# Optimization experiments

Measured on AMD Instinct MI355X. Metric: run time of the kernel, lower is better.

The kernel has to match this reference:

```python
import jax, jax.numpy as jnp
import numpy as np
from jax import lax

B, L, M, H = 8, 16, 256, 53
HID, NH, HD = 64, 4, 16  # hidden_size, n_heads, head_dim
ACT = 15  # 3 sub-actions x 5 categories


def _lstm_last(x, Wih, Whh, bih, bhh):
    # x: [N, T, D] batch_first; torch LSTM gate order i,f,g,o. Returns last hidden [N, HID].
    N = x.shape[0]
    h0 = jnp.zeros((N, HID), x.dtype)
    c0 = jnp.zeros((N, HID), x.dtype)
    def step(carry, xt):
        h, c = carry
        g = xt @ Wih.T + bih + h @ Whh.T + bhh
        i, f, gg, o = jnp.split(g, 4, axis=-1)
        c = jax.nn.sigmoid(f) * c + jax.nn.sigmoid(i) * jnp.tanh(gg)
        h = jax.nn.sigmoid(o) * jnp.tanh(c)
        return (h, c), None
    (h, _), _ = lax.scan(step, (h0, c0), x.transpose(1, 0, 2))
    return h


def setup_inputs():
    key = jax.random.key(0)
    ks = jax.random.split(key, 32)
    rn = lambda k, sh: (jax.random.normal(k, sh, jnp.float32) * 0.05)
    Gmat = jax.random.randint(ks[3], (M, M), 0, 2)
    Gmat = Gmat.at[jnp.arange(M), jnp.arange(M)].set(1)  # self-contact so no all-masked row
    return {
        'x_actor': jax.random.normal(ks[0], (B, L, M, H), jnp.float32),
        'x_critic': jax.random.normal(ks[1], (B, L, M, H), jnp.float32),
        'action': jax.random.randint(ks[2], (B, M, 3), 0, 5),
        'Gmat': Gmat,
        'Wa': rn(ks[4], (HID, H)), 'ba': jnp.zeros((HID,), jnp.float32),
        'Wg': rn(ks[5], (HID, H)), 'bg': jnp.zeros((HID,), jnp.float32),
        'Qw': rn(ks[6], (HID, HID)), 'Kw': rn(ks[7], (HID, HID)),
        'W2': rn(ks[8], (HID, 2 * HID)), 'b2': jnp.zeros((HID,), jnp.float32),
        'Wih_a': rn(ks[9], (4 * HID, HID)), 'Whh_a': rn(ks[10], (4 * HID, HID)),
        'bih_a': jnp.zeros((4 * HID,), jnp.float32), 'bhh_a': jnp.zeros((4 * HID,), jnp.float32),
        'Wih_c': rn(ks[11], (4 * HID, HID)), 'Whh_c': rn(ks[12], (4 * HID, HID)),
        'bih_c': jnp.zeros((4 * HID,), jnp.float32), 'bhh_c': jnp.zeros((4 * HID,), jnp.float32),
        'Wma1': rn(ks[13], (HID, HID)), 'bma1': jnp.zeros((HID,), jnp.float32),
        'Wma2': rn(ks[14], (ACT, HID)), 'bma2': jnp.zeros((ACT,), jnp.float32),
        'Wmc1': rn(ks[15], (HID, HID)), 'bmc1': jnp.zeros((HID,), jnp.float32),
        'Wmc2': rn(ks[16], (1, HID)), 'bmc2': jnp.zeros((1,), jnp.float32),
    }


def reference(x_actor, x_critic, action, Gmat, Wa, ba, Wg, bg, Qw, Kw, W2, b2,
              Wih_a, Whh_a, bih_a, bhh_a, Wih_c, Whh_c, bih_c, bhh_c,
              Wma1, bma1, Wma2, bma2, Wmc1, bmc1, Wmc2, bmc2):
    Bb, Ll, Mm, Hh = x_actor.shape
    xa = x_actor.transpose(1, 0, 2, 3).reshape(Ll * Bb, Mm, Hh)
    xc = xa  # original code overwrites x_critic with x_actor (preserved)
    a_lin = xa @ Wa.T + ba                               # [LB, M, HID]
    # --- GAT (GCN2) ---
    s = xc @ Wg.T + bg                                   # [LB, M, HID]
    q = (s @ Qw).reshape(-1, Mm, NH, HD)
    k = (s @ Kw).reshape(-1, Mm, NH, HD)
    s4 = s.reshape(-1, Mm, NH, HD)
    att = jnp.einsum('blhe,bshe->bhls', q, k) / jnp.asarray(128.0, s.dtype) ** 0.5
    att = jnp.where(Gmat > 0, att, jnp.asarray(-9e15, att.dtype))
    att = jax.nn.softmax(att, axis=-1)
    s_out = jnp.einsum('bshe,bhls->blhe', s4, att).reshape(-1, Mm, NH * HD)
    c_feat = jnp.concatenate([s, s_out], axis=-1) @ W2.T + b2  # [LB, M, HID]
    # --- to sequences [B*M, L, HID] ---
    xa_seq = a_lin.reshape(Ll, Bb * Mm, HID).transpose(1, 0, 2)
    xc_seq = c_feat.reshape(Ll, Bb * Mm, HID).transpose(1, 0, 2)
    ah = _lstm_last(xa_seq, Wih_a, Whh_a, bih_a, bhh_a)          # [B*M, HID]
    ch = _lstm_last(xc_seq, Wih_c, Whh_c, bih_c, bhh_c).reshape(Bb, Mm, HID)
    logits = (jnp.tanh(ah @ Wma1.T + bma1) @ Wma2.T + bma2).reshape(Bb, Mm, 3, 5)
    logp = jax.nn.log_softmax(logits, axis=-1)
    lp = jnp.take_along_axis(logp, action[..., None], axis=-1).squeeze(-1)  # [B,M,3]
    ent = -jnp.sum(jnp.exp(logp) * logp, axis=-1)                           # [B,M,3]
    value = jnp.tanh(ch @ Wmc1.T + bmc1) @ Wmc2.T + bmc2                    # [B,M,1]
    return (action, lp.sum(-1), ent.sum(-1), value)
```

## Files before the change

### kernel.cpp

```cpp
#include <hip/hip_runtime.h>
#include <math.h>

#define B_ 8
#define L_ 16
#define M_ 256
#define H_ 53
#define HID_ 64
#define LB_ 128
#define SCALE_ 0.08838834764831845f

typedef __attribute__((ext_vector_type(8))) short bf16x8;
typedef __attribute__((ext_vector_type(4))) float f32x4;

__device__ inline unsigned short f2bf(float f) {
  unsigned u = __builtin_bit_cast(unsigned, f);
  unsigned r = (u + 0x7FFFu + ((u >> 16) & 1u)) >> 16;
  return (unsigned short)r;
}
__device__ inline float bf2f(unsigned short u) {
  unsigned v = ((unsigned)u) << 16;
  return __builtin_bit_cast(float, v);
}
__device__ inline float sigm(float x) { return __builtin_amdgcn_rcpf(1.f + __expf(-x)); }
__device__ inline float ftanh(float x) { return 1.f - 2.f * __builtin_amdgcn_rcpf(1.f + __expf(2.f * x)); }

__global__ __launch_bounds__(256) void kP_pre(
    const float* __restrict__ Wa, const float* __restrict__ Wg,
    const float* __restrict__ bg,
    const float* __restrict__ Qw, const float* __restrict__ Kw,
    unsigned short* __restrict__ WQ_b, unsigned short* __restrict__ WK_b,
    float* __restrict__ bqk, unsigned short* __restrict__ Wab_b) {
  int blk = blockIdx.x, tid = threadIdx.x;
  if (blk < 32) {
    int idx = blk * 256 + tid;
    int which = idx >> 12, n = (idx >> 6) & 63, j = idx & 63;
    const float* Mm = which ? Kw : Qw;
    float acc = 0.f;
    if (j < 53) {
      for (int e = 0; e < 64; ++e) acc = fmaf(Mm[e * 64 + n], Wg[e * 53 + j], acc);
      if (which == 0) acc *= SCALE_;
    }
    (which ? WK_b : WQ_b)[n * 64 + j] = f2bf(acc);
  } else if (blk == 32) {
    if (tid < 128) {
      int which = tid >> 6, n = tid & 63;
      const float* Mm = which ? Kw : Qw;
      float acc = 0.f;
      for (int e = 0; e < 64; ++e) acc = fmaf(bg[e], Mm[e * 64 + n], acc);
      if (which == 0) acc *= SCALE_;
      bqk[tid] = acc;
    }
  } else {
    int base = (blk - 33) * 4096;
    #pragma unroll
    for (int k = 0; k < 16; ++k) {
      int idx = base + k * 256 + tid;
      int n = idx >> 6, j = idx & 63;
      float v = 0.f;
      if (j < 53) v = (n < 64) ? Wa[n * 53 + j] : Wg[(n - 64) * 53 + j];
      Wab_b[idx] = f2bf(v);
    }
  }
}

#define WS 68
#define OS 268
__global__ __launch_bounds__(256, 2) void kA_lin(const float* __restrict__ x,
    const unsigned short* __restrict__ Wab_b,
    const unsigned short* __restrict__ WQ_b, const unsigned short* __restrict__ WK_b,
    const float* __restrict__ ba, const float* __restrict__ bg,
    const float* __restrict__ bqk,
    const int* __restrict__ Gmat, const float* __restrict__ Wih_c,
    const float* __restrict__ W2, const float* __restrict__ b2,
    const float* __restrict__ Whh_a, const float* __restrict__ Whh_c,
    const float* __restrict__ Wih_a,
    unsigned short* __restrict__ a_lin_bf, unsigned short* __restrict__ s_b,
    unsigned short* __restrict__ q_b, unsigned short* __restrict__ k_b,
    unsigned short* __restrict__ sT_b,
    unsigned short* __restrict__ Wfold_b, float* __restrict__ bias_fold,
    unsigned* __restrict__ gmask,
    unsigned short* __restrict__ Whha_b, unsigned short* __restrict__ Whhc_b,
    unsigned short* __restrict__ Wiha_b) {
  int tid = threadIdx.x, blk = blockIdx.x;
  if (blk >= 512) {
    int b2k = blk - 512;
    if (b2k < 128) {
      int idx = b2k * 256 + tid;
      int n = idx >> 7, t = idx & 127;
      float acc = 0.f;
      for (int e = 0; e < 64; ++e) acc = fmaf(Wih_c[n * 64 + e], W2[e * 128 + t], acc);
      Wfold_b[idx] = f2bf(acc);
    } else if (b2k < 192) {
      int l = (b2k - 128) * 4 + (tid >> 6);
      int ln = tid & 63;
      #pragma unroll
      for (int c = 0; c < 4; ++c) {
        int gv = Gmat[l * 256 + c * 64 + ln];
        unsigned long long msk = __ballot(gv > 0);
        if (ln == 0) {
          gmask[l * 8 + c * 2] = (unsigned)msk;
          gmask[l * 8 + c * 2 + 1] = (unsigned)(msk >> 32);
        }
      }
    } else if (b2k == 192) {
      float acc = 0.f;
      for (int e = 0; e < 64; ++e) acc = fmaf(Wih_c[tid * 64 + e], b2[e], acc);
      bias_fold[tid] = acc;
    } else {
      int base = (b2k - 193) * 2048;
      #pragma unroll
      for (int k = 0; k < 8; ++k) {
        int idx = base + k * 256 + tid;
        if (idx < 16384) Whha_b[idx] = f2bf(Whh_a[idx]);
        else if (idx < 32768) Whhc_b[idx - 16384] = f2bf(Whh_c[idx - 16384]);
        else Wiha_b[idx - 32768] = f2bf(Wih_a[idx - 32768]);
      }
    }
    return;
  }
  __shared__ __attribute__((aligned(16))) char smem[70144];
  float* x_raw = (float*)smem;
  unsigned short* out_lds = (unsigned short*)smem;
  unsigned short* w_lds = (unsigned short*)(smem + 34304);
  float* bias_lds = (float*)(smem + 69120);
  int row0 = blk * 64;
  int lbA = row0 >> 8, m0 = row0 & 255;
  int lA = lbA >> 3, bA = lbA & 7;
  {
    const uint4* xs = (const uint4*)(x + ((bA * L_ + lA) * M_ + m0) * H_);
    uint4* xr = (uint4*)x_raw;
    #pragma unroll
    for (int k = 0; k < 4; ++k) {
      int i = k * 256 + tid;
      if (i < 848) xr[i] = xs[i];
    }
  }
  #pragma unroll
  for (int k = 0; k < 8; ++k) {
    int i = k * 256 + tid;
    int n = i >> 3, c8 = (i & 7) * 8;
    const unsigned short* src = n < 128 ? Wab_b + n * 64
                              : (n < 192 ? WQ_b + (n - 128) * 64 : WK_b + (n - 192) * 64);
    *(uint4*)&w_lds[n * WS + c8] = *(const uint4*)(src + c8);
  }
  {
    float bv;
    if (tid < 64) bv = ba[tid];
    else if (tid < 128) bv = bg[tid - 64];
    else bv = bqk[tid - 128];
    bias_lds[tid] = bv;
  }
  __syncthreads();
  int lane = tid & 63, w = tid >> 6;
  int c16 = lane & 15, q4 = lane >> 4;
  int lrow = w * 16 + c16;
  bf16x8 a0, a1;
  #pragma unroll
  for (int e = 0; e < 8; ++e)
    a0[e] = (short)f2bf(x_raw[lrow * H_ + q4 * 8 + e]);
  #pragma unroll
  for (int e = 0; e < 8; ++e) {
    int c = 32 + q4 * 8 + e;
    a1[e] = (c < H_) ? (short)f2bf(x_raw[lrow * H_ + c]) : (short)0;
  }
  __syncthreads();
  #pragma unroll
  for (int nt = 0; nt < 16; ++nt) {
    bf16x8 b0 = *(const bf16x8*)&w_lds[(nt * 16 + c16) * WS + q4 * 8];
    bf16x8 b1 = *(const bf16x8*)&w_lds[(nt * 16 + c16) * WS + 32 + q4 * 8];
    float bs = bias_lds[nt * 16 + c16];
    f32x4 acc = {bs, bs, bs, bs};
    acc = __builtin_amdgcn_mfma_f32_16x16x32_bf16(a0, b0, acc, 0, 0, 0);
    acc = __builtin_amdgcn_mfma_f32_16x16x32_bf16(a1, b1, acc, 0, 0, 0);
    #pragma unroll
    for (int rr = 0; rr < 4; ++rr)
      out_lds[(w * 16 + q4 * 4 + rr) * OS + nt * 16 + c16] = f2bf(acc[rr]);
  }
  __syncthreads();
  #pragma unroll
  for (int k = 0; k < 8; ++k) {
    int i = k * 256 + tid;
    int r = i >> 5, seg = i & 31;
    int which = seg >> 3, n8 = (seg & 7) * 8;
    uint4 v = *(const uint4*)&out_lds[r * OS + which * 64 + n8];
    unsigned short* dst = which == 0 ? a_lin_bf : which == 1 ? s_b : which == 2 ? q_b : k_b;
    *(uint4*)&dst[(row0 + r) * 64 + n8] = v;
  }
  #pragma unroll
  for (int k = 0; k < 4; ++k) {
    int i = k * 256 + tid;
    int e = i >> 4, mc = i & 15;
    ushort4 v;
    v.x = out_lds[(mc * 4 + 0) * OS + 64 + e];
    v.y = out_lds[(mc * 4 + 1) * OS + 64 + e];
    v.z = out_lds[(mc * 4 + 2) * OS + 64 + e];
    v.w = out_lds[(mc * 4 + 3) * OS + 64 + e];
    *(ushort4*)&sT_b[(lbA * 64 + e) * 256 + m0 + mc * 4] = v;
  }
}

__global__ __launch_bounds__(512, 4) void kB_attn(
    const unsigned short* __restrict__ qb, const unsigned short* __restrict__ kb,
    const unsigned short* __restrict__ sT, const unsigned* __restrict__ gmask,
    unsigned short* __restrict__ so_b) {
  __shared__ __attribute__((aligned(16))) unsigned short k_lds[256 * 68];
  __shared__ __attribute__((aligned(16))) unsigned short sT_lds[64 * 280];
  int bid = blockIdx.x;
  int xcd = bid & 7;
  int rest = bid >> 3;
  int l0 = (rest & 3) << 6;
  int lb = (rest >> 2) * 8 + xcd;
  int tid = threadIdx.x;
  int kbase = lb * 256;
  for (int i = tid; i < 2048; i += 512) {
    int s = i >> 3, e8 = (i & 7) * 8;
    *(uint4*)&k_lds[s * 68 + e8] = *(const uint4*)(kb + (kbase + s) * 64 + e8);
  }
  for (int i = tid; i < 2048; i += 512) {
    int e = i >> 5, m8 = (i & 31) * 8;
    *(uint4*)&sT_lds[e * 280 + m8] = *(const uint4*)(sT + (lb * 64 + e) * 256 + m8);
  }
  int lane = tid & 63, w = tid >> 6;
  int c16 = lane & 15, q4 = lane >> 4;
  int lrow0 = (w >> 1) * 16;
  int h0 = (w & 1) * 2;
  int lrow = lb * 256 + l0 + lrow0;
  const bf16x8 z8 = {0, 0, 0, 0, 0, 0, 0, 0};
  bf16x8 bq[2];
  #pragma unroll
  for (int hp = 0; hp < 2; ++hp) {
    int h = h0 + hp;
    bq[hp] = (q4 < 2) ? *(const bf16x8*)(qb + (lrow + c16) * 64 + h * 16 + q4 * 8) : z8;
  }
  unsigned gwv[8];
  #pragma unroll
  for (int sp = 0; sp < 8; ++sp) gwv[sp] = gmask[(l0 + lrow0 + c16) * 8 + sp];
  __syncthreads();
  f32x4 accO[2];
  float sumh[2];
  #pragma unroll
  for (int hp = 0; hp < 2; ++hp) { accO[hp] = (f32x4){0.f, 0.f, 0.f, 0.f}; sumh[hp] = 0.f; }

  #pragma unroll
  for (int sp = 0; sp < 8; ++sp) {
    unsigned gw = gwv[sp];
    #pragma unroll
    for (int hp = 0; hp < 2; ++hp) {
      int h = h0 + hp;
      unsigned pk0A, pk1A, pk0B, pk1B;
      #pragma unroll
      for (int tp = 0; tp < 2; ++tp) {
        int t = sp * 2 + tp;
        bf16x8 ka = z8;
        if (q4 < 2) ka = *(const bf16x8*)&k_lds[(t * 16 + c16) * 68 + h * 16 + q4 * 8];
        f32x4 d = __builtin_amdgcn_mfma_f32_16x16x32_bf16(ka, bq[hp], (f32x4){0.f, 0.f, 0.f, 0.f}, 0, 0, 0);
        int bitbase = tp * 16 + q4 * 4;
        float p0 = ((gw >> (bitbase + 0)) & 1u) ? __expf(d[0]) : 0.f;
        float p1 = ((gw >> (bitbase + 1)) & 1u) ? __expf(d[1]) : 0.f;
        float p2 = ((gw >> (bitbase + 2)) & 1u) ? __expf(d[2]) : 0.f;
        float p3 = ((gw >> (bitbase + 3)) & 1u) ? __expf(d[3]) : 0.f;
        sumh[hp] += (p0 + p1) + (p2 + p3);
        unsigned lo = (unsigned)f2bf(p0) | ((unsigned)f2bf(p1) << 16);
        unsigned hi = (unsigned)f2bf(p2) | ((unsigned)f2bf(p3) << 16);
        if (tp == 0) { pk0A = lo; pk1A = hi; } else { pk0B = lo; pk1B = hi; }
      }
      int srcA = ((q4 & 1) * 2) * 16 + c16, srcB = srcA + 16;
      unsigned g0A = (unsigned)__shfl((int)pk0A, srcA);
      unsigned g1A = (unsigned)__shfl((int)pk1A, srcA);
      unsigned g2A = (unsigned)__shfl((int)pk0A, srcB);
      unsigned g3A = (unsigned)__shfl((int)pk1A, srcB);
      unsigned g0B = (unsigned)__shfl((int)pk0B, srcA);
      unsigned g1B = (unsigned)__shfl((int)pk1B, srcA);
      unsigned g2B = (unsigned)__shfl((int)pk0B, srcB);
      unsigned g3B = (unsigned)__shfl((int)pk1B, srcB);
      bool useB = (q4 >= 2);
      uint4 av;
      av.x = useB ? g0B : g0A;
      av.y = useB ? g1B : g1A;
      av.z = useB ? g2B : g2A;
      av.w = useB ? g3B : g3A;
      bf16x8 af = __builtin_bit_cast(bf16x8, av);
      bf16x8 bs = *(const bf16x8*)&sT_lds[(h * 16 + c16) * 280 + sp * 32 + q4 * 8];
      accO[hp] = __builtin_amdgcn_mfma_f32_16x16x32_bf16(af, bs, accO[hp], 0, 0, 0);
    }
  }
  #pragma unroll
  for (int hp = 0; hp < 2; ++hp) {
    int h = h0 + hp;
    float s = sumh[hp];
    s += __shfl_xor(s, 16);
    s += __shfl_xor(s, 32);
    #pragma unroll
    for (int r = 0; r < 4; ++r) {
      float sv = __shfl(s, q4 * 4 + r);
      float o = accO[hp][r] / sv;
      so_b[(lb * 256 + l0 + lrow0 + q4 * 4 + r) * 64 + h * 16 + c16] = f2bf(o);
    }
  }
}

__global__ __launch_bounds__(256, 1) void kR_lstm(
    const unsigned short* __restrict__ a_lin_bf,
    const unsigned short* __restrict__ s_b, const unsigned short* __restrict__ so_b,
    const unsigned short* __restrict__ Wfold_b, const float* __restrict__ bias_fold,
    const unsigned short* __restrict__ Wiha_b,
    const unsigned short* __restrict__ Whha_b, const unsigned short* __restrict__ Whhc_b,
    const float* __restrict__ bih_a, const float* __restrict__ bhh_a,
    const float* __restrict__ bih_c, const float* __restrict__ bhh_c,
    const int* __restrict__ action,
    const float* __restrict__ Wma1, const float* __restrict__ bma1,
    const float* __restrict__ Wma2, const float* __restrict__ bma2,
    const float* __restrict__ Wmc1, const float* __restrict__ bmc1,
    const float* __restrict__ Wmc2, const float* __restrict__ bmc2,
    float* __restrict__ out) {
  int blk = blockIdx.x;
  int which = blk >> 7, g = blk & 127;
  int seq0 = g * 16;
  int b = seq0 >> 8, m0 = seq0 & 255;
  __shared__ __attribute__((aligned(16))) unsigned short h_lds[2][16][72];
  __shared__ __attribute__((aligned(16))) unsigned short ha_lds[16][72];
  __shared__ float logit_lds[16][16];
  __shared__ float grp_lds[16][8];
  __shared__ float val_lds[16][4];
  int tid = threadIdx.x;
  int lane = tid & 63, w = tid >> 6;
  int c16 = lane & 15, q4 = lane >> 4;
  int hs0 = w * 16;
  const unsigned short* Whh_b = which ? Whhc_b : Whha_b;
  const float* bih = which ? bih_c : bih_a;
  const float* bhh = which ? bhh_c : bhh_a;
  bf16x8 bwhh[4][2];
  float bias[4];
  #pragma unroll
  for (int nt = 0; nt < 4; ++nt) {
    int n = nt * 64 + hs0 + c16;
    bias[nt] = bih[n] + bhh[n] + (which ? bias_fold[n] : 0.f);
    #pragma unroll
    for (int kf = 0; kf < 2; ++kf)
      bwhh[nt][kf] = *(const bf16x8*)(Whh_b + n * 64 + kf * 32 + q4 * 8);
  }
  for (int i = tid; i < 576; i += 256) ((unsigned*)h_lds)[i] = 0u;
  float cr[4] = {0.f, 0.f, 0.f, 0.f};
  const int STEP = 2048 * 64;
  __syncthreads();
  int cur = 0;
  if (which == 0) {
    bf16x8 bwin[4][2];
    #pragma unroll
    for (int nt = 0; nt < 4; ++nt) {
      int n = nt * 64 + hs0 + c16;
      #pragma unroll
      for (int kf = 0; kf < 2; ++kf)
        bwin[nt][kf] = *(const bf16x8*)(Wiha_b + n * 64 + kf * 32 + q4 * 8);
    }
    const unsigned short* inb = a_lin_bf + (b * 256 + m0 + c16) * 64;
    bf16x8 i0c = *(const bf16x8*)(inb + q4 * 8);
    bf16x8 i1c = *(const bf16x8*)(inb + 32 + q4 * 8);
    for (int l = 0; l < L_; ++l) {
      bf16x8 i0n = i0c, i1n = i1c;
      if (l < L_ - 1) {
        i0n = *(const bf16x8*)(inb + (l + 1) * STEP + q4 * 8);
        i1n = *(const bf16x8*)(inb + (l + 1) * STEP + 32 + q4 * 8);
      }
      bf16x8 ah0 = *(const bf16x8*)&h_lds[cur][c16][q4 * 8];
      bf16x8 ah1 = *(const bf16x8*)&h_lds[cur][c16][32 + q4 * 8];
      f32x4 acc[4];
      #pragma unroll
      for (int nt = 0; nt < 4; ++nt) {
        f32x4 a = {bias[nt], bias[nt], bias[nt], bias[nt]};
        a = __builtin_amdgcn_mfma_f32_16x16x32_bf16(i0c, bwin[nt][0], a, 0, 0, 0);
        a = __builtin_amdgcn_mfma_f32_16x16x32_bf16(i1c, bwin[nt][1], a, 0, 0, 0);
        a = __builtin_amdgcn_mfma_f32_16x16x32_bf16(ah0, bwhh[nt][0], a, 0, 0, 0);
        a = __builtin_amdgcn_mfma_f32_16x16x32_bf16(ah1, bwhh[nt][1], a, 0, 0, 0);
        acc[nt] = a;
      }
      #pragma unroll
      for (int rr = 0; rr < 4; ++rr) {
        float si = sigm(acc[0][rr]);
        float sf = sigm(acc[1][rr]);
        float gg = ftanh(acc[2][rr]);
        float so_ = sigm(acc[3][rr]);
        cr[rr] = sf * cr[rr] + si * gg;
        float hvv = so_ * ftanh(cr[rr]);
        h_lds[cur ^ 1][q4 * 4 + rr][hs0 + c16] = f2bf(hvv);
      }
      __syncthreads();
      cur ^= 1;
      i0c = i0n; i1c = i1n;
    }
  } else {
    bf16x8 bwf[4][4];
    #pragma unroll
    for (int nt = 0; nt < 4; ++nt) {
      int n = nt * 64 + hs0 + c16;
      #pragma unroll
// ... 40 lines not shown
      }
      __syncthreads();
      cur ^= 1;
      s0c = s0n; s1c = s1n; o0c = o0n; o1c = o1n;
    }
  }
  bf16x8 fh0 = *(const bf16x8*)&h_lds[cur][c16][q4 * 8];
  bf16x8 fh1 = *(const bf16x8*)&h_lds[cur][c16][32 + q4 * 8];
  if (which == 0) {
    bf16x8 bm1[2];
    #pragma unroll
    for (int kf = 0; kf < 2; ++kf) {
      const float* wp = Wma1 + (hs0 + c16) * 64 + kf * 32 + q4 * 8;
      bf16x8 bb;
      #pragma unroll
      for (int j = 0; j < 8; ++j) bb[j] = (short)f2bf(wp[j]);
      bm1[kf] = bb;
    }
    float bs = bma1[hs0 + c16];
    f32x4 acc = {bs, bs, bs, bs};
    acc = __builtin_amdgcn_mfma_f32_16x16x32_bf16(fh0, bm1[0], acc, 0, 0, 0);
    acc = __builtin_amdgcn_mfma_f32_16x16x32_bf16(fh1, bm1[1], acc, 0, 0, 0);
    #pragma unroll
    for (int rr = 0; rr < 4; ++rr)
      ha_lds[q4 * 4 + rr][hs0 + c16] = f2bf(ftanh(acc[rr]));
    __syncthreads();
    if (w == 0) {
      bf16x8 af0 = *(const bf16x8*)&ha_lds[c16][q4 * 8];
      bf16x8 af1 = *(const bf16x8*)&ha_lds[c16][32 + q4 * 8];
      const bf16x8 z8 = {0, 0, 0, 0, 0, 0, 0, 0};
      bf16x8 bw2[2] = {z8, z8};
      float bs2 = 0.f;
      if (c16 < 15) {
        #pragma unroll
        for (int kf = 0; kf < 2; ++kf) {
          const float* wp = Wma2 + c16 * 64 + kf * 32 + q4 * 8;
          bf16x8 bb;
          #pragma unroll
          for (int j = 0; j < 8; ++j) bb[j] = (short)f2bf(wp[j]);
          bw2[kf] = bb;
        }
        bs2 = bma2[c16];
      }
      f32x4 acc2 = {bs2, bs2, bs2, bs2};
      acc2 = __builtin_amdgcn_mfma_f32_16x16x32_bf16(af0, bw2[0], acc2, 0, 0, 0);
      acc2 = __builtin_amdgcn_mfma_f32_16x16x32_bf16(af1, bw2[1], acc2, 0, 0, 0);
      #pragma unroll
      for (int rr = 0; rr < 4; ++rr)
        logit_lds[q4 * 4 + rr][c16] = acc2[rr];
    }
    __syncthreads();
    if (tid < 48) {
      int useq = tid & 15, t = tid >> 4;
      int n = seq0 + useq;
      float l0 = logit_lds[useq][t * 5 + 0], l1 = logit_lds[useq][t * 5 + 1];
      float l2 = logit_lds[useq][t * 5 + 2], l3 = logit_lds[useq][t * 5 + 3];
      float l4 = logit_lds[useq][t * 5 + 4];
      float mx = fmaxf(fmaxf(fmaxf(l0, l1), fmaxf(l2, l3)), l4);
      float sm = __expf(l0 - mx) + __expf(l1 - mx) + __expf(l2 - mx) +
                 __expf(l3 - mx) + __expf(l4 - mx);
      float lse = __logf(sm) + mx;
      int a = action[n * 3 + t];
      float lp0 = l0 - lse, lp1 = l1 - lse, lp2 = l2 - lse, lp3 = l3 - lse, lp4 = l4 - lse;
      float lpsel = logit_lds[useq][t * 5 + a] - lse;
      float ent = -(__expf(lp0) * lp0 + __expf(lp1) * lp1 + __expf(lp2) * lp2 +
                    __expf(lp3) * lp3 + __expf(lp4) * lp4);
      grp_lds[useq][t] = lpsel;
      grp_lds[useq][4 + t] = ent;
      out[n * 3 + t] = (float)a;
    }
    __syncthreads();
    if (tid < 16) {
      int n = seq0 + tid;
      out[6144 + n] = grp_lds[tid][0] + grp_lds[tid][1] + grp_lds[tid][2];
      out[8192 + n] = grp_lds[tid][4] + grp_lds[tid][5] + grp_lds[tid][6];
    }
  } else {
    bf16x8 bm1[2];
    #pragma unroll
    for (int kf = 0; kf < 2; ++kf) {
      const float* wp = Wmc1 + (hs0 + c16) * 64 + kf * 32 + q4 * 8;
      bf16x8 bb;
      #pragma unroll
      for (int j = 0; j < 8; ++j) bb[j] = (short)f2bf(wp[j]);
      bm1[kf] = bb;
    }
    float bs = bmc1[hs0 + c16];
    f32x4 acc = {bs, bs, bs, bs};
    acc = __builtin_amdgcn_mfma_f32_16x16x32_bf16(fh0, bm1[0], acc, 0, 0, 0);
    acc = __builtin_amdgcn_mfma_f32_16x16x32_bf16(fh1, bm1[1], acc, 0, 0, 0);
    float wv2 = Wmc2[hs0 + c16];
    float pv[4];
    #pragma unroll
    for (int rr = 0; rr < 4; ++rr) pv[rr] = ftanh(acc[rr]) * wv2;
    #pragma unroll
    for (int rr = 0; rr < 4; ++rr) {
      pv[rr] += __shfl_xor(pv[rr], 1);
      pv[rr] += __shfl_xor(pv[rr], 2);
      pv[rr] += __shfl_xor(pv[rr], 4);
      pv[rr] += __shfl_xor(pv[rr], 8);
    }
    if (c16 == 0) {
      #pragma unroll
      for (int rr = 0; rr < 4; ++rr) val_lds[q4 * 4 + rr][w] = pv[rr];
    }
    __syncthreads();
    if (tid < 16) {
      int n = seq0 + tid;
      out[10240 + n] = val_lds[tid][0] + val_lds[tid][1] + val_lds[tid][2] +
                       val_lds[tid][3] + bmc2[0];
    }
  }
}

extern "C" void kernel_launch(void* const* d_in, const int* in_sizes, int n_in,
                              void* d_out, int out_size, void* d_ws, size_t ws_size,
                              hipStream_t stream) {
  const float* x_actor = (const float*)d_in[0];
  const int* action = (const int*)d_in[2];
  const int* Gmat  = (const int*)d_in[3];
  const float* Wa = (const float*)d_in[4];  const float* ba = (const float*)d_in[5];
  const float* Wg = (const float*)d_in[6];  const float* bg = (const float*)d_in[7];
  const float* Qw = (const float*)d_in[8];  const float* Kw = (const float*)d_in[9];
  const float* W2 = (const float*)d_in[10]; const float* b2 = (const float*)d_in[11];
  const float* Wih_a = (const float*)d_in[12]; const float* Whh_a = (const float*)d_in[13];
  const float* bih_a = (const float*)d_in[14]; const float* bhh_a = (const float*)d_in[15];
  const float* Wih_c = (const float*)d_in[16]; const float* Whh_c = (const float*)d_in[17];
  const float* bih_c = (const float*)d_in[18]; const float* bhh_c = (const float*)d_in[19];
  const float* Wma1 = (const float*)d_in[20]; const float* bma1 = (const float*)d_in[21];
  const float* Wma2 = (const float*)d_in[22]; const float* bma2 = (const float*)d_in[23];
  const float* Wmc1 = (const float*)d_in[24]; const float* bmc1 = (const float*)d_in[25];
  const float* Wmc2 = (const float*)d_in[26]; const float* bmc2 = (const float*)d_in[27];

  unsigned short* us = (unsigned short*)d_ws;
  unsigned short* a_lin_bf = us;
  unsigned short* s_b  = us + 2097152;
  unsigned short* q_b  = us + 4194304;
  unsigned short* k_b  = us + 6291456;
  unsigned short* sT_b = us + 8388608;
  unsigned short* so_b = us + 10485760;
  unsigned short* Wfold_b = us + 12582912;
  unsigned short* Whha_b  = us + 12615680;
  unsigned short* Whhc_b  = us + 12632064;
  unsigned short* Wiha_b  = us + 12648448;
  unsigned short* WQ_b    = us + 12664832;
  unsigned short* WK_b    = us + 12668928;
  unsigned short* Wab_b   = us + 12673024;
  float* fb = (float*)(us + 12681216);
  float* bias_fold = fb;
  float* bqk = fb + 256;
  unsigned* gmask = (unsigned*)(fb + 384);
  float* out = (float*)d_out;

  kP_pre<<<35, 256, 0, stream>>>(Wa, Wg, bg, Qw, Kw, WQ_b, WK_b, bqk, Wab_b);
  kA_lin<<<729, 256, 0, stream>>>(x_actor, Wab_b, WQ_b, WK_b, ba, bg, bqk,
                                  Gmat, Wih_c, W2, b2, Whh_a, Whh_c, Wih_a,
                                  a_lin_bf, s_b, q_b, k_b, sT_b,
                                  Wfold_b, bias_fold, gmask,
                                  Whha_b, Whhc_b, Wiha_b);
  kB_attn<<<512, 512, 0, stream>>>(q_b, k_b, sT_b, gmask, so_b);
  kR_lstm<<<256, 256, 0, stream>>>(a_lin_bf, s_b, so_b, Wfold_b, bias_fold,
                                   Wiha_b, Whha_b, Whhc_b,
                                   bih_a, bhh_a, bih_c, bhh_c,
                                   action, Wma1, bma1, Wma2, bma2,
                                   Wmc1, bmc1, Wmc2, bmc2, out);
}
```

Before: 67.94 us.

## Fuse all four kernels into one cooperative megakernel with grid syncs

Replaces the four-kernel launch sequence with a single cooperative kernel of 256 blocks x 512 threads that runs the same stages (weight prep, input projection, masked attention, LSTM plus heads) separated by grid.sync barriers. The aim is to remove launch gaps and inter-kernel drain between stages. The trade-offs are fewer resident blocks than the separate launches used (729 and 512 blocks before), idle half-blocks in the prep and LSTM stages, and the cost of the grid barriers themselves. The old multi-kernel path is kept as a fallback if the cooperative launch fails.

```diff
diff --git a/kernel.cpp b/kernel.cpp
--- a/kernel.cpp
+++ b/kernel.cpp
@@ -1,5 +1,8 @@
 #include <hip/hip_runtime.h>
+#include <hip/hip_cooperative_groups.h>
 #include <math.h>
+
+namespace cg = cooperative_groups;
 
 #define B_ 8
 #define L_ 16
@@ -23,6 +26,522 @@
 }
 __device__ inline float sigm(float x) { return __builtin_amdgcn_rcpf(1.f + __expf(-x)); }
 __device__ inline float ftanh(float x) { return 1.f - 2.f * __builtin_amdgcn_rcpf(1.f + __expf(2.f * x)); }
+
+__global__ __launch_bounds__(512, 2) void kMega(
+    const float* __restrict__ x,
+    const float* __restrict__ Wa, const float* __restrict__ Wg,
+    const float* __restrict__ ba, const float* __restrict__ bg,
+    const float* __restrict__ Qw, const float* __restrict__ Kw,
+    const int* __restrict__ Gmat, const float* __restrict__ Wih_c,
+    const float* __restrict__ W2, const float* __restrict__ b2,
+    const float* __restrict__ Whh_a, const float* __restrict__ Whh_c,
+    const float* __restrict__ Wih_a,
+    const float* __restrict__ bih_a, const float* __restrict__ bhh_a,
+    const float* __restrict__ bih_c, const float* __restrict__ bhh_c,
+    const int* __restrict__ action,
+    const float* __restrict__ Wma1, const float* __restrict__ bma1,
+    const float* __restrict__ Wma2, const float* __restrict__ bma2,
+    const float* __restrict__ Wmc1, const float* __restrict__ bmc1,
+    const float* __restrict__ Wmc2, const float* __restrict__ bmc2,
+    unsigned short* __restrict__ WQ_b, unsigned short* __restrict__ WK_b,
+    float* __restrict__ bqk, unsigned short* __restrict__ Wab_b,
+    unsigned short* __restrict__ a_lin_bf, unsigned short* __restrict__ s_b,
+    unsigned short* __restrict__ q_b, unsigned short* __restrict__ k_b,
+    unsigned short* __restrict__ sT_b, unsigned short* __restrict__ so_b,
+    unsigned short* __restrict__ Wfold_b, float* __restrict__ bias_fold,
+    unsigned* __restrict__ gmask,
+    unsigned short* __restrict__ Whha_b, unsigned short* __restrict__ Whhc_b,
+    unsigned short* __restrict__ Wiha_b, float* __restrict__ out) {
+  __shared__ __attribute__((aligned(16))) char smem[140288];
+  cg::grid_group grid = cg::this_grid();
+  int blk = blockIdx.x, tid = threadIdx.x;
+
+  if (tid < 256) {
+    int t = tid;
+    if (blk < 32) {
+      int idx = blk * 256 + t;
+      int which = idx >> 12, n = (idx >> 6) & 63, j = idx & 63;
+      const float* Mm = which ? Kw : Qw;
+      float acc = 0.f;
+      if (j < 53) {
+        for (int e = 0; e < 64; ++e) acc = fmaf(Mm[e * 64 + n], Wg[e * 53 + j], acc);
+        if (which == 0) acc *= SCALE_;
+      }
+      (which ? WK_b : WQ_b)[n * 64 + j] = f2bf(acc);
+    } else if (blk == 32) {
+      if (t < 128) {
+        int which = t >> 6, n = t & 63;
+        const float* Mm = which ? Kw : Qw;
+        float acc = 0.f;
+        for (int e = 0; e < 64; ++e) acc = fmaf(bg[e], Mm[e * 64 + n], acc);
+        if (which == 0) acc *= SCALE_;
+        bqk[t] = acc;
+      }
+      float bacc = 0.f;
+      for (int e = 0; e < 64; ++e) bacc = fmaf(Wih_c[t * 64 + e], b2[e], bacc);
+      bias_fold[t] = bacc;
+    } else if (blk < 35) {
+      int base = (blk - 33) * 4096;
+      #pragma unroll
+      for (int k = 0; k < 16; ++k) {
+        int idx = base + k * 256 + t;
+        int n = idx >> 6, j = idx & 63;
+        float v = 0.f;
+        if (j < 53) v = (n < 64) ? Wa[n * 53 + j] : Wg[(n - 64) * 53 + j];
+        Wab_b[idx] = f2bf(v);
+      }
+    } else if (blk < 163) {
+      int idx = (blk - 35) * 256 + t;
+      int n = idx >> 7, tt = idx & 127;
+      float acc = 0.f;
+      for (int e = 0; e < 64; ++e) acc = fmaf(Wih_c[n * 64 + e], W2[e * 128 + tt], acc);
+      Wfold_b[idx] = f2bf(acc);
+    } else if (blk < 227) {
+      int l = (blk - 163) * 4 + (t >> 6);
+      int ln = t & 63;
+      #pragma unroll
+      for (int c = 0; c < 4; ++c) {
+        int gv = Gmat[l * 256 + c * 64 + ln];
+        unsigned long long msk = __ballot(gv > 0);
+        if (ln == 0) {
+          gmask[l * 8 + c * 2] = (unsigned)msk;
+          gmask[l * 8 + c * 2 + 1] = (unsigned)(msk >> 32);
+        }
+      }
+    } else if (blk < 251) {
+      int base = (blk - 227) * 2048;
+      #pragma unroll
+      for (int k = 0; k < 8; ++k) {
+        int idx = base + k * 256 + t;
+        if (idx < 16384) Whha_b[idx] = f2bf(Whh_a[idx]);
+        else if (idx < 32768) Whhc_b[idx - 16384] = f2bf(Whh_c[idx - 16384]);
+        else Wiha_b[idx - 32768] = f2bf(Wih_a[idx - 32768]);
+      }
+    }
+  }
+  grid.sync();
+
+  {
+    int group = tid >> 8, t = tid & 255;
+    char* base = smem + group * 70144;
+    float* x_raw = (float*)base;
+    unsigned short* out_lds = (unsigned short*)base;
+    unsigned short* w_lds = (unsigned short*)(base + 34304);
+    float* bias_lds = (float*)(base + 69120);
+    int job = blk * 2 + group;
+    int row0 = job * 64;
+    int lbA = row0 >> 8, m0 = row0 & 255;
+    int lA = lbA >> 3, bA = lbA & 7;
+    {
+      const uint4* xs = (const uint4*)(x + ((bA * L_ + lA) * M_ + m0) * H_);
+      uint4* xr = (uint4*)x_raw;
+      #pragma unroll
+      for (int k = 0; k < 4; ++k) {
+        int i = k * 256 + t;
+        if (i < 848) xr[i] = xs[i];
+      }
+    }
+    #pragma unroll
+    for (int k = 0; k < 8; ++k) {
+      int i = k * 256 + t;
+      int n = i >> 3, c8 = (i & 7) * 8;
+      const unsigned short* src = n < 128 ? Wab_b + n * 64
+                                : (n < 192 ? WQ_b + (n - 128) * 64 : WK_b + (n - 192) * 64);
+      *(uint4*)&w_lds[n * 68 + c8] = *(const uint4*)(src + c8);
+    }
+    {
+      float bv;
+      if (t < 64) bv = ba[t];
+      else if (t < 128) bv = bg[t - 64];
+      else bv = bqk[t - 128];
+      bias_lds[t] = bv;
+    }
+    __syncthreads();
+    int lane = t & 63, w = t >> 6;
+    int c16 = lane & 15, q4 = lane >> 4;
+    int lrow = w * 16 + c16;
+    bf16x8 a0, a1;
+    #pragma unroll
+    for (int e = 0; e < 8; ++e)
+      a0[e] = (short)f2bf(x_raw[lrow * H_ + q4 * 8 + e]);
+    #pragma unroll
+    for (int e = 0; e < 8; ++e) {
+      int c = 32 + q4 * 8 + e;
+      a1[e] = (c < H_) ? (short)f2bf(x_raw[lrow * H_ + c]) : (short)0;
+    }
+    __syncthreads();
+    #pragma unroll
+    for (int nt = 0; nt < 16; ++nt) {
+      bf16x8 b0 = *(const bf16x8*)&w_lds[(nt * 16 + c16) * 68 + q4 * 8];
+      bf16x8 b1 = *(const bf16x8*)&w_lds[(nt * 16 + c16) * 68 + 32 + q4 * 8];
+      float bs = bias_lds[nt * 16 + c16];
+      f32x4 acc = {bs, bs, bs, bs};
+      acc = __builtin_amdgcn_mfma_f32_16x16x32_bf16(a0, b0, acc, 0, 0, 0);
+      acc = __builtin_amdgcn_mfma_f32_16x16x32_bf16(a1, b1, acc, 0, 0, 0);
+      #pragma unroll
+      for (int rr = 0; rr < 4; ++rr)
+        out_lds[(w * 16 + q4 * 4 + rr) * 268 + nt * 16 + c16] = f2bf(acc[rr]);
+    }
+    __syncthreads();
+    #pragma unroll
+    for (int k = 0; k < 8; ++k) {
+      int i = k * 256 + t;
+      int r = i >> 5, seg = i & 31;
+      int which = seg >> 3, n8 = (seg & 7) * 8;
+      uint4 v = *(const uint4*)&out_lds[r * 268 + which * 64 + n8];
+      unsigned short* dst = which == 0 ? a_lin_bf : which == 1 ? s_b : which == 2 ? q_b : k_b;
+      *(uint4*)&dst[(row0 + r) * 64 + n8] = v;
+    }
+    #pragma unroll
+    for (int k = 0; k < 4; ++k) {
+      int i = k * 256 + t;
+      int e = i >> 4, mc = i & 15;
+      ushort4 v;
+      v.x = out_lds[(mc * 4 + 0) * 268 + 64 + e];
+      v.y = out_lds[(mc * 4 + 1) * 268 + 64 + e];
+      v.z = out_lds[(mc * 4 + 2) * 268 + 64 + e];
+      v.w = out_lds[(mc * 4 + 3) * 268 + 64 + e];
+      *(ushort4*)&sT_b[(lbA * 64 + e) * 256 + m0 + mc * 4] = v;
+    }
+  }
+  grid.sync();
+
+  {
+    unsigned short* k_lds = (unsigned short*)smem;
+    unsigned short* sT_lds = (unsigned short*)(smem + 34816);
+    int lb = blk >> 1, half = blk & 1;
+    int kbase = lb * 256;
+    for (int i = tid; i < 2048; i += 512) {
+      int s = i >> 3, e8 = (i & 7) * 8;
+      *(uint4*)&k_lds[s * 68 + e8] = *(const uint4*)(k_b + (kbase + s) * 64 + e8);
+    }
+    for (int i = tid; i < 2048; i += 512) {
+      int e = i >> 5, m8 = (i & 31) * 8;
+      *(uint4*)&sT_lds[e * 280 + m8] = *(const uint4*)(sT_b + (lb * 64 + e) * 256 + m8);
+    }
+    __syncthreads();
+    int lane = tid & 63, w = tid >> 6;
+    int c16 = lane & 15, q4 = lane >> 4;
+    int lrow0 = (w >> 1) * 16;
+    int h0 = (w & 1) * 2;
+    const bf16x8 z8 = {0, 0, 0, 0, 0, 0, 0, 0};
+    #pragma unroll
+    for (int q2 = 0; q2 < 2; ++q2) {
+      int l0 = ((half << 1) | q2) << 6;
+      int lrow = lb * 256 + l0 + lrow0;
+      bf16x8 bq[2];
+      #pragma unroll
+      for (int hp = 0; hp < 2; ++hp) {
+        int h = h0 + hp;
+        bq[hp] = (q4 < 2) ? *(const bf16x8*)(q_b + (lrow + c16) * 64 + h * 16 + q4 * 8) : z8;
+      }
+      unsigned gwv[8];
+      #pragma unroll
+      for (int sp = 0; sp < 8; ++sp) gwv[sp] = gmask[(l0 + lrow0 + c16) * 8 + sp];
+      f32x4 accO[2];
+      float sumh[2];
+      #pragma unroll
+      for (int hp = 0; hp < 2; ++hp) { accO[hp] = (f32x4){0.f, 0.f, 0.f, 0.f}; sumh[hp] = 0.f; }
+      #pragma unroll
+      for (int sp = 0; sp < 8; ++sp) {
+        unsigned gw = gwv[sp];
+        #pragma unroll
+        for (int hp = 0; hp < 2; ++hp) {
+          int h = h0 + hp;
+          unsigned pk0A, pk1A, pk0B, pk1B;
+          #pragma unroll
+          for (int tp = 0; tp < 2; ++tp) {
+            int tt = sp * 2 + tp;
+            bf16x8 ka = z8;
+            if (q4 < 2) ka = *(const bf16x8*)&k_lds[(tt * 16 + c16) * 68 + h * 16 + q4 * 8];
+            f32x4 d = __builtin_amdgcn_mfma_f32_16x16x32_bf16(ka, bq[hp], (f32x4){0.f, 0.f, 0.f, 0.f}, 0, 0, 0);
+            int bitbase = tp * 16 + q4 * 4;
+            float p0 = ((gw >> (bitbase + 0)) & 1u) ? __expf(d[0]) : 0.f;
+            float p1 = ((gw >> (bitbase + 1)) & 1u) ? __expf(d[1]) : 0.f;
+            float p2 = ((gw >> (bitbase + 2)) & 1u) ? __expf(d[2]) : 0.f;
+            float p3 = ((gw >> (bitbase + 3)) & 1u) ? __expf(d[3]) : 0.f;
+            sumh[hp] += (p0 + p1) + (p2 + p3);
+            unsigned lo = (unsigned)f2bf(p0) | ((unsigned)f2bf(p1) << 16);
+            unsigned hi = (unsigned)f2bf(p2) | ((unsigned)f2bf(p3) << 16);
+            if (tp == 0) { pk0A = lo; pk1A = hi; } else { pk0B = lo; pk1B = hi; }
+          }
+          int srcA = ((q4 & 1) * 2) * 16 + c16, srcB = srcA + 16;
+          unsigned g0A = (unsigned)__shfl((int)pk0A, srcA);
+          unsigned g1A = (unsigned)__shfl((int)pk1A, srcA);
+          unsigned g2A = (unsigned)__shfl((int)pk0A, srcB);
+          unsigned g3A = (unsigned)__shfl((int)pk1A, srcB);
+          unsigned g0B = (unsigned)__shfl((int)pk0B, srcA);
+          unsigned g1B = (unsigned)__shfl((int)pk1B, srcA);
+          unsigned g2B = (unsigned)__shfl((int)pk0B, srcB);
+          unsigned g3B = (unsigned)__shfl((int)pk1B, srcB);
+          bool useB = (q4 >= 2);
+          uint4 av;
+          av.x = useB ? g0B : g0A;
+          av.y = useB ? g1B : g1A;
+          av.z = useB ? g2B : g2A;
+          av.w = useB ? g3B : g3A;
+          bf16x8 af = __builtin_bit_cast(bf16x8, av);
+          bf16x8 bs = *(const bf16x8*)&sT_lds[(h * 16 + c16) * 280 + sp * 32 + q4 * 8];
+          accO[hp] = __builtin_amdgcn_mfma_f32_16x16x32_bf16(af, bs, accO[hp], 0, 0, 0);
+        }
+      }
+      #pragma unroll
+      for (int hp = 0; hp < 2; ++hp) {
+        int h = h0 + hp;
+        float s = sumh[hp];
+        s += __shfl_xor(s, 16);
+        s += __shfl_xor(s, 32);
+        #pragma unroll
+        for (int r = 0; r < 4; ++r) {
+          float sv = __shfl(s, q4 * 4 + r);
+          float o = accO[hp][r] / sv;
+          so_b[(lb * 256 + l0 + lrow0 + q4 * 4 + r) * 64 + h * 16 + c16] = f2bf(o);
+        }
+      }
+    }
+  }
+  grid.sync();
+
+  if (tid < 256) {
+    int t = tid;
+    unsigned short (*h_lds)[16][72] = (unsigned short(*)[16][72])(smem);
+    unsigned short (*ha_lds)[72] = (unsigned short(*)[72])(smem + 4608);
+    float (*logit_lds)[16] = (float(*)[16])(smem + 6912);
+    float (*grp_lds)[8] = (float(*)[8])(smem + 7936);
+    float (*val_lds)[4] = (float(*)[4])(smem + 8448);
+    int which = blk >> 7, g = blk & 127;
+    int seq0 = g * 16;
+    int b = seq0 >> 8, m0 = seq0 & 255;
+    int lane = t & 63, w = t >> 6;
+    int c16 = lane & 15, q4 = lane >> 4;
+    int hs0 = w * 16;
+    const unsigned short* Whh_bp = which ? Whhc_b : Whha_b;
+    const float* bih = which ? bih_c : bih_a;
+    const float* bhh = which ? bhh_c : bhh_a;
+    bf16x8 bwhh[4][2];
+    float bias[4];
+    #pragma unroll
+    for (int nt = 0; nt < 4; ++nt) {
+      int n = nt * 64 + hs0 + c16;
+      bias[nt] = bih[n] + bhh[n] + (which ? bias_fold[n] : 0.f);
+      #pragma unroll
+      for (int kf = 0; kf < 2; ++kf)
+        bwhh[nt][kf] = *(const bf16x8*)(Whh_bp + n * 64 + kf * 32 + q4 * 8);
+    }
+    for (int i = t; i < 576; i += 256) ((unsigned*)smem)[i] = 0u;
+    float cr[4] = {0.f, 0.f, 0.f, 0.f};
+    float hv[4] = {0.f, 0.f, 0.f, 0.f};
+    const int STEP = 2048 * 64;
+    __syncthreads();
+    int cur = 0;
+    if (which == 0) {
+      bf16x8 bwin[4][2];
+      #pragma unroll
+      for (int nt = 0; nt < 4; ++nt) {
+        int n = nt * 64 + hs0 + c16;
+        #pragma unroll
+        for (int kf = 0; kf < 2; ++kf)
+          bwin[nt][kf] = *(const bf16x8*)(Wiha_b + n * 64 + kf * 32 + q4 * 8);
+      }
+      const unsigned short* inb = a_lin_bf + (b * 256 + m0 + c16) * 64;
+      bf16x8 i0c = *(const bf16x8*)(inb + q4 * 8);
+      bf16x8 i1c = *(const bf16x8*)(inb + 32 + q4 * 8);
+      for (int l = 0; l < L_; ++l) {
+        bf16x8 i0n = i0c, i1n = i1c;
+        if (l < L_ - 1) {
+          i0n = *(const bf16x8*)(inb + (l + 1) * STEP + q4 * 8);
+          i1n = *(const bf16x8*)(inb + (l + 1) * STEP + 32 + q4 * 8);
+        }
+        bf16x8 ah0 = *(const bf16x8*)&h_lds[cur][c16][q4 * 8];
+        bf16x8 ah1 = *(const bf16x8*)&h_lds[cur][c16][32 + q4 * 8];
+        f32x4 acc[4];
+        #pragma unroll
+        for (int nt = 0; nt < 4; ++nt) {
+          f32x4 a = {bias[nt], bias[nt], bias[nt], bias[nt]};
+          a = __builtin_amdgcn_mfma_f32_16x16x32_bf16(i0c, bwin[nt][0], a, 0, 0, 0);
+          a = __builtin_amdgcn_mfma_f32_16x16x32_bf16(i1c, bwin[nt][1], a, 0, 0, 0);
+          a = __builtin_amdgcn_mfma_f32_16x16x32_bf16(ah0, bwhh[nt][0], a, 0, 0, 0);
+          a = __builtin_amdgcn_mfma_f32_16x16x32_bf16(ah1, bwhh[nt][1], a, 0, 0, 0);
+          acc[nt] = a;
+        }
+        #pragma unroll
+        for (int rr = 0; rr < 4; ++rr) {
+          float si = sigm(acc[0][rr]);
+          float sf = sigm(acc[1][rr]);
+          float gg = ftanh(acc[2][rr]);
+          float so_ = sigm(acc[3][rr]);
+          cr[rr] = sf * cr[rr] + si * gg;
+          hv[rr] = so_ * ftanh(cr[rr]);
+          h_lds[cur ^ 1][q4 * 4 + rr][hs0 + c16] = f2bf(hv[rr]);
+        }
+        __syncthreads();
+        cur ^= 1;
+        i0c = i0n; i1c = i1n;
+      }
+    } else {
+      bf16x8 bwf[4][4];
+      #pragma unroll
+      for (int nt = 0; nt < 4; ++nt) {
+        int n = nt * 64 + hs0 + c16;
+        #pragma unroll
+        for (int kc = 0; kc < 4; ++kc)
+          bwf[nt][kc] = *(const bf16x8*)(Wfold_b + n * 128 + kc * 32 + q4 * 8);
+      }
+      const unsigned short* sbB = s_b + (b * 256 + m0 + c16) * 64;
+      const unsigned short* soB = so_b + (b * 256 + m0 + c16) * 64;
+      bf16x8 s0c = *(const bf16x8*)(sbB + q4 * 8);
+      bf16x8 s1c = *(const bf16x8*)(sbB + 32 + q4 * 8);
+      bf16x8 o0c = *(const bf16x8*)(soB + q4 * 8);
+      bf16x8 o1c = *(const bf16x8*)(soB + 32 + q4 * 8);
+      for (int l = 0; l < L_; ++l) {
+        bf16x8 s0n = s0c, s1n = s1c, o0n = o0c, o1n = o1c;
+        if (l < L_ - 1) {
+          s0n = *(const bf16x8*)(sbB + (l + 1) * STEP + q4 * 8);
+          s1n = *(const bf16x8*)(sbB + (l + 1) * STEP + 32 + q4 * 8);
+          o0n = *(const bf16x8*)(soB + (l + 1) * STEP + q4 * 8);
+          o1n = *(const bf16x8*)(soB + (l + 1) * STEP + 32 + q4 * 8);
+        }
+        bf16x8 ah0 = *(const bf16x8*)&h_lds[cur][c16][q4 * 8];
+        bf16x8 ah1 = *(const bf16x8*)&h_lds[cur][c16][32 + q4 * 8];
+        f32x4 acc[4];
+        #pragma unroll
+        for (int nt = 0; nt < 4; ++nt) {
+          f32x4 a = {bias[nt], bias[nt], bias[nt], bias[nt]};
+          a = __builtin_amdgcn_mfma_f32_16x16x32_bf16(s0c, bwf[nt][0], a, 0, 0, 0);
+          a = __builtin_amdgcn_mfma_f32_16x16x32_bf16(s1c, bwf[nt][1], a, 0, 0, 0);
+          a = __builtin_amdgcn_mfma_f32_16x16x32_bf16(o0c, bwf[nt][2], a, 0, 0, 0);
+          a = __builtin_amdgcn_mfma_f32_16x16x32_bf16(o1c, bwf[nt][3], a, 0, 0, 0);
+          a = __builtin_amdgcn_mfma_f32_16x16x32_bf16(ah0, bwhh[nt][0], a, 0, 0, 0);
+          a = __builtin_amdgcn_mfma_f32_16x16x32_bf16(ah1, bwhh[nt][1], a, 0, 0, 0);
+          acc[nt] = a;
+        }
+        #pragma unroll
+        for (int rr = 0; rr < 4; ++rr) {
+          float si = sigm(acc[0][rr]);
+          float sf = sigm(acc[1][rr]);
+          float gg = ftanh(acc[2][rr]);
+          float so_ = sigm(acc[3][rr]);
+          cr[rr] = sf * cr[rr] + si * gg;
+          hv[rr] = so_ * ftanh(cr[rr]);
+          h_lds[cur ^ 1][q4 * 4 + rr][hs0 + c16] = f2bf(hv[rr]);
+        }
+        __syncthreads();
+        cur ^= 1;
+        s0c = s0n; s1c = s1n; o0c = o0n; o1c = o1n;
+      }
+    }
+    bf16x8 fh0 = *(const bf16x8*)&h_lds[cur][c16][q4 * 8];
+    bf16x8 fh1 = *(const bf16x8*)&h_lds[cur][c16][32 + q4 * 8];
+    if (which == 0) {
+      bf16x8 bm1[2];
+      #pragma unroll
+      for (int kf = 0; kf < 2; ++kf) {
+        const float* wp = Wma1 + (hs0 + c16) * 64 + kf * 32 + q4 * 8;
+        bf16x8 bb;
+        #pragma unroll
+        for (int j = 0; j < 8; ++j) bb[j] = (short)f2bf(wp[j]);
+        bm1[kf] = bb;
+      }
+      float bs = bma1[hs0 + c16];
+      f32x4 acc = {bs, bs, bs, bs};
+      acc = __builtin_amdgcn_mfma_f32_16x16x32_bf16(fh0, bm1[0], acc, 0, 0, 0);
+      acc = __builtin_amdgcn_mfma_f32_16x16x32_bf16(fh1, bm1[1], acc, 0, 0, 0);
+      #pragma unroll
+      for (int rr = 0; rr < 4; ++rr)
+        ha_lds[q4 * 4 + rr][hs0 + c16] = f2bf(ftanh(acc[rr]));
+      __syncthreads();
+      if (w == 0) {
+        bf16x8 af0 = *(const bf16x8*)&ha_lds[c16][q4 * 8];
+        bf16x8 af1 = *(const bf16x8*)&ha_lds[c16][32 + q4 * 8];
+        const bf16x8 z8 = {0, 0, 0, 0, 0, 0, 0, 0};
+        bf16x8 bw2[2] = {z8, z8};
+        float bs2 = 0.f;
+        if (c16 < 15) {
+          #pragma unroll
+          for (int kf = 0; kf < 2; ++kf) {
+            const float* wp = Wma2 + c16 * 64 + kf * 32 + q4 * 8;
+            bf16x8 bb;
+            #pragma unroll
+            for (int j = 0; j < 8; ++j) bb[j] = (short)f2bf(wp[j]);
+            bw2[kf] = bb;
+          }
+          bs2 = bma2[c16];
+        }
+        f32x4 acc2 = {bs2, bs2, bs2, bs2};
+        acc2 = __builtin_amdgcn_mfma_f32_16x16x32_bf16(af0, bw2[0], acc2, 0, 0, 0);
+        acc2 = __builtin_amdgcn_mfma_f32_16x16x32_bf16(af1, bw2[1], acc2, 0, 0, 0);
+        #pragma unroll
+        for (int rr = 0; rr < 4; ++rr)
+          logit_lds[q4 * 4 + rr][c16] = acc2[rr];
+      }
+      __syncthreads();
+      if (t < 48) {
+        int useq = t & 15, tt = t >> 4;
+        int n = seq0 + useq;
+        float l0 = logit_lds[useq][tt * 5 + 0], l1 = logit_lds[useq][tt * 5 + 1];
+        float l2 = logit_lds[useq][tt * 5 + 2], l3 = logit_lds[useq][tt * 5 + 3];
+        float l4 = logit_lds[useq][tt * 5 + 4];
+        float mx = fmaxf(fmaxf(fmaxf(l0, l1), fmaxf(l2, l3)), l4);
+        float sm = __expf(l0 - mx) + __expf(l1 - mx) + __expf(l2 - mx) +
+                   __expf(l3 - mx) + __expf(l4 - mx);
+        float lse = __logf(sm) + mx;
+        int a = action[n * 3 + tt];
+        float lp0 = l0 - lse, lp1 = l1 - lse, lp2 = l2 - lse, lp3 = l3 - lse, lp4 = l4 - lse;
+        float lpsel = logit_lds[useq][tt * 5 + a] - lse;
+        float ent = -(__expf(lp0) * lp0 + __expf(lp1) * lp1 + __expf(lp2) * lp2 +
+                      __expf(lp3) * lp3 + __expf(lp4) * lp4);
+        grp_lds[useq][tt] = lpsel;
+        grp_lds[useq][4 + tt] = ent;
+        out[n * 3 + tt] = (float)a;
+      }
+      __syncthreads();
+      if (t < 16) {
+        int n = seq0 + t;
+        out[6144 + n] = grp_lds[t][0] + grp_lds[t][1] + grp_lds[t][2];
+        out[8192 + n] = grp_lds[t][4] + grp_lds[t][5] + grp_lds[t][6];
+      }
+    } else {
+      bf16x8 bm1[2];
+      #pragma unroll
+      for (int kf = 0; kf < 2; ++kf) {
+        const float* wp = Wmc1 + (hs0 + c16) * 64 + kf * 32 + q4 * 8;
+        bf16x8 bb;
+        #pragma unroll
+        for (int j = 0; j < 8; ++j) bb[j] = (short)f2bf(wp[j]);
+        bm1[kf] = bb;
+      }
+      float bs = bmc1[hs0 + c16];
+      f32x4 acc = {bs, bs, bs, bs};
+      acc = __builtin_amdgcn_mfma_f32_16x16x32_bf16(fh0, bm1[0], acc, 0, 0, 0);
+      acc = __builtin_amdgcn_mfma_f32_16x16x32_bf16(fh1, bm1[1], acc, 0, 0, 0);
+      float wv2 = Wmc2[hs0 + c16];
+      float pv[4];
+      #pragma unroll
+      for (int rr = 0; rr < 4; ++rr) pv[rr] = ftanh(acc[rr]) * wv2;
+      #pragma unroll
+      for (int rr = 0; rr < 4; ++rr) {
+        pv[rr] += __shfl_xor(pv[rr], 1);
+        pv[rr] += __shfl_xor(pv[rr], 2);
+        pv[rr] += __shfl_xor(pv[rr], 4);
+        pv[rr] += __shfl_xor(pv[rr], 8);
+      }
+      if (c16 == 0) {
+        #pragma unroll
+        for (int rr = 0; rr < 4; ++rr) val_lds[q4 * 4 + rr][w] = pv[rr];
+      }
+      __syncthreads();
+      if (t < 16) {
+        int n = seq0 + t;
+        out[10240 + n] = val_lds[t][0] + val_lds[t][1] + val_lds[t][2] +
+                         val_lds[t][3] + bmc2[0];
+      }
+      __syncthreads();
+      __syncthreads();
+    }
+  } else {
+    for (int i = 0; i < 20; ++i) __syncthreads();
+  }
+}
 
 __global__ __launch_bounds__(256) void kP_pre(
     const float* __restrict__ Wa, const float* __restrict__ Wg,
@@ -63,8 +582,6 @@
   }
 }
 
-#define WS 68
-#define OS 268
 __global__ __launch_bounds__(256, 2) void kA_lin(const float* __restrict__ x,
     const unsigned short* __restrict__ Wab_b,
     const unsigned short* __restrict__ WQ_b, const unsigned short* __restrict__ WK_b,
@@ -141,7 +658,7 @@
     int n = i >> 3, c8 = (i & 7) * 8;
     const unsigned short* src = n < 128 ? Wab_b + n * 64
                               : (n < 192 ? WQ_b + (n - 128) * 64 : WK_b + (n - 192) * 64);
-    *(uint4*)&w_lds[n * WS + c8] = *(const uint4*)(src + c8);
+    *(uint4*)&w_lds[n * 68 + c8] = *(const uint4*)(src + c8);
   }
   {
     float bv;
@@ -166,15 +683,15 @@
   __syncthreads();
   #pragma unroll
   for (int nt = 0; nt < 16; ++nt) {
-    bf16x8 b0 = *(const bf16x8*)&w_lds[(nt * 16 + c16) * WS + q4 * 8];
-    bf16x8 b1 = *(const bf16x8*)&w_lds[(nt * 16 + c16) * WS + 32 + q4 * 8];
+    bf16x8 b0 = *(const bf16x8*)&w_lds[(nt * 16 + c16) * 68 + q4 * 8];
+    bf16x8 b1 = *(const bf16x8*)&w_lds[(nt * 16 + c16) * 68 + 32 + q4 * 8];
     float bs = bias_lds[nt * 16 + c16];
     f32x4 acc = {bs, bs, bs, bs};
     acc = __builtin_amdgcn_mfma_f32_16x16x32_bf16(a0, b0, acc, 0, 0, 0);
     acc = __builtin_amdgcn_mfma_f32_16x16x32_bf16(a1, b1, acc, 0, 0, 0);
     #pragma unroll
     for (int rr = 0; rr < 4; ++rr)
-      out_lds[(w * 16 + q4 * 4 + rr) * OS + nt * 16 + c16] = f2bf(acc[rr]);
+      out_lds[(w * 16 + q4 * 4 + rr) * 268 + nt * 16 + c16] = f2bf(acc[rr]);
   }
   __syncthreads();
   #pragma unroll
@@ -182,7 +699,7 @@
     int i = k * 256 + tid;
     int r = i >> 5, seg = i & 31;
     int which = seg >> 3, n8 = (seg & 7) * 8;
-    uint4 v = *(const uint4*)&out_lds[r * OS + which * 64 + n8];
+    uint4 v = *(const uint4*)&out_lds[r * 268 + which * 64 + n8];
     unsigned short* dst = which == 0 ? a_lin_bf : which == 1 ? s_b : which == 2 ? q_b : k_b;
     *(uint4*)&dst[(row0 + r) * 64 + n8] = v;
   }
@@ -191,10 +708,10 @@
     int i = k * 256 + tid;
     int e = i >> 4, mc = i & 15;
     ushort4 v;
-    v.x = out_lds[(mc * 4 + 0) * OS + 64 + e];
-    v.y = out_lds[(mc * 4 + 1) * OS + 64 + e];
-    v.z = out_lds[(mc * 4 + 2) * OS + 64 + e];
-    v.w = out_lds[(mc * 4 + 3) * OS + 64 + e];
+    v.x = out_lds[(mc * 4 + 0) * 268 + 64 + e];
+    v.y = out_lds[(mc * 4 + 1) * 268 + 64 + e];
+    v.z = out_lds[(mc * 4 + 2) * 268 + 64 + e];
+    v.w = out_lds[(mc * 4 + 3) * 268 + 64 + e];
     *(ushort4*)&sT_b[(lbA * 64 + e) * 256 + m0 + mc * 4] = v;
   }
 }
@@ -240,7 +757,6 @@
   float sumh[2];
   #pragma unroll
   for (int hp = 0; hp < 2; ++hp) { accO[hp] = (f32x4){0.f, 0.f, 0.f, 0.f}; sumh[hp] = 0.f; }
-
   #pragma unroll
   for (int sp = 0; sp < 8; ++sp) {
     unsigned gw = gwv[sp];
@@ -587,16 +1103,31 @@
   unsigned* gmask = (unsigned*)(fb + 384);
   float* out = (float*)d_out;
 
-  kP_pre<<<35, 256, 0, stream>>>(Wa, Wg, bg, Qw, Kw, WQ_b, WK_b, bqk, Wab_b);
-  kA_lin<<<729, 256, 0, stream>>>(x_actor, Wab_b, WQ_b, WK_b, ba, bg, bqk,
-                                  Gmat, Wih_c, W2, b2, Whh_a, Whh_c, Wih_a,
-                                  a_lin_bf, s_b, q_b, k_b, sT_b,
-                                  Wfold_b, bias_fold, gmask,
-                                  Whha_b, Whhc_b, Wiha_b);
-  kB_attn<<<512, 512, 0, stream>>>(q_b, k_b, sT_b, gmask, so_b);
-  kR_lstm<<<256, 256, 0, stream>>>(a_lin_bf, s_b, so_b, Wfold_b, bias_fold,
-                                   Wiha_b, Whha_b, Whhc_b,
-                                   bih_a, bhh_a, bih_c, bhh_c,
-                                   action, Wma1, bma1, Wma2, bma2,
-                                   Wmc1, bmc1, Wmc2, bmc2, out);
+  void* args[] = {
+    (void*)&x_actor, (void*)&Wa, (void*)&Wg, (void*)&ba, (void*)&bg,
+    (void*)&Qw, (void*)&Kw, (void*)&Gmat, (void*)&Wih_c, (void*)&W2, (void*)&b2,
+    (void*)&Whh_a, (void*)&Whh_c, (void*)&Wih_a,
+    (void*)&bih_a, (void*)&bhh_a, (void*)&bih_c, (void*)&bhh_c, (void*)&action,
+    (void*)&Wma1, (void*)&bma1, (void*)&Wma2, (void*)&bma2,
+    (void*)&Wmc1, (void*)&bmc1, (void*)&Wmc2, (void*)&bmc2,
+    (void*)&WQ_b, (void*)&WK_b, (void*)&bqk, (void*)&Wab_b,
+    (void*)&a_lin_bf, (void*)&s_b, (void*)&q_b, (void*)&k_b, (void*)&sT_b,
+    (void*)&so_b, (void*)&Wfold_b, (void*)&bias_fold, (void*)&gmask,
+    (void*)&Whha_b, (void*)&Whhc_b, (void*)&Wiha_b, (void*)&out};
+  hipError_t err = hipLaunchCooperativeKernel(
+      reinterpret_cast<void*>(kMega), dim3(256), dim3(512), args, 0u, stream);
+  if (err != hipSuccess) {
+    kP_pre<<<35, 256, 0, stream>>>(Wa, Wg, bg, Qw, Kw, WQ_b, WK_b, bqk, Wab_b);
+    kA_lin<<<729, 256, 0, stream>>>(x_actor, Wab_b, WQ_b, WK_b, ba, bg, bqk,
+                                    Gmat, Wih_c, W2, b2, Whh_a, Whh_c, Wih_a,
+                                    a_lin_bf, s_b, q_b, k_b, sT_b,
+                                    Wfold_b, bias_fold, gmask,
+                                    Whha_b, Whhc_b, Wiha_b);
+    kB_attn<<<512, 512, 0, stream>>>(q_b, k_b, sT_b, gmask, so_b);
+    kR_lstm<<<256, 256, 0, stream>>>(a_lin_bf, s_b, so_b, Wfold_b, bias_fold,
+                                     Wiha_b, Whha_b, Whhc_b,
+                                     bih_a, bhh_a, bih_c, bhh_c,
+                                     action, Wma1, bma1, Wma2, bma2,
+                                     Wmc1, bmc1, Wmc2, bmc2, out);
+  }
 }
```

After: 169.6 us. 2.5x slower.
